# Optimization experiments

Hardware: AMD Instinct MI355X
Metric: run time of the kernel (lower is better)

## Reference

```python
import jax, jax.numpy as jnp
import numpy as np

N = 100_000      # nodes per type
E = 1_000_000    # edges per edge type
F_IN = 32        # raw feature dim
HID = 64         # hidden_channels
H, D = 2, 32     # num_heads, head_dim


def setup_inputs() -> dict:
    key = jax.random.key(0)
    ks = jax.random.split(key, 64)
    it = iter(range(64))
    def nrm(shape, scale=0.1):
        return jax.random.normal(ks[next(it)], shape, dtype=jnp.float32) * scale
    inp = {}
    inp['x_mac'] = jax.random.normal(ks[next(it)], (N, F_IN), dtype=jnp.float32)
    inp['x_buf'] = jax.random.normal(ks[next(it)], (N, F_IN), dtype=jnp.float32)
    inp['ei_m2b'] = jax.random.randint(ks[next(it)], (2, E), 0, N)
    inp['ei_b2m'] = jax.random.randint(ks[next(it)], (2, E), 0, N)
    for t in ('mac', 'buf'):
        inp[f'enc_w_{t}'] = nrm((F_IN, HID))
        inp[f'enc_b_{t}'] = jnp.zeros((HID,), jnp.float32)
        inp[f'enc_g_{t}'] = jnp.ones((HID,), jnp.float32)
        inp[f'enc_be_{t}'] = jnp.zeros((HID,), jnp.float32)
        for p in ('k', 'q', 'v'):
            inp[f'{p}_w_{t}'] = nrm((HID, HID))
            inp[f'{p}_b_{t}'] = jnp.zeros((HID,), jnp.float32)
        inp[f'o_w_{t}'] = nrm((HID, HID))
        inp[f'o_b_{t}'] = jnp.zeros((HID,), jnp.float32)
        inp[f'skip_{t}'] = jnp.ones((), jnp.float32)
    for r in ('m2b', 'b2m'):
        inp[f'a_{r}'] = nrm((H, D, D))
        inp[f'm_{r}'] = nrm((H, D, D))
        inp[f'p_{r}'] = jnp.ones((H,), jnp.float32)
    inp['ln_g'] = jnp.ones((HID,), jnp.float32)
    inp['ln_b'] = jnp.zeros((HID,), jnp.float32)
    return inp


def _ln(x, g, b, eps=1e-5):
    mu = jnp.mean(x, -1, keepdims=True)
    var = jnp.mean((x - mu) ** 2, -1, keepdims=True)
    return g * (x - mu) * jax.lax.rsqrt(var + eps) + b


def _seg_softmax(logits, seg, n):
    # logits: [E, H], seg: [E] dst ids. Numerically stable per-segment softmax.
    m = jax.ops.segment_max(logits, seg, num_segments=n)
    m = jnp.where(jnp.isfinite(m), m, 0.0)  # empty segments -> -inf
    e = jnp.exp(logits - m[seg])
    s = jax.ops.segment_sum(e, seg, num_segments=n)
    return e / (s[seg] + 1e-16)


def _hgt_edge(q_dst, k_src, v_src, a_rel, m_rel, p_rel, ei, n_dst):
    # q_dst:[Nd,H,D] k_src/v_src:[Ns,H,D] a_rel/m_rel:[H,D,D] p_rel:[H] ei:[2,E]
    src, dst = ei[0], ei[1]
    k = jnp.einsum('nhd,hde->nhe', k_src, a_rel)   # relation-transform keys
    v = jnp.einsum('nhd,hde->nhe', v_src, m_rel)   # relation-transform values
    alpha = (q_dst[dst] * k[src]).sum(-1) * p_rel / jnp.sqrt(jnp.float32(D))  # [E,H]
    alpha = _seg_softmax(alpha, dst, n_dst)
    msg = v[src] * alpha[..., None]                # [E,H,D]
    return jax.ops.segment_sum(msg, dst, num_segments=n_dst).reshape(n_dst, H * D)


def _forward(x_mac, x_buf, ei_m2b, ei_b2m,
             enc_w_mac, enc_b_mac, enc_g_mac, enc_be_mac,
             enc_w_buf, enc_b_buf, enc_g_buf, enc_be_buf,
             k_w_mac, k_b_mac, q_w_mac, q_b_mac, v_w_mac, v_b_mac,
             k_w_buf, k_b_buf, q_w_buf, q_b_buf, v_w_buf, v_b_buf,
             o_w_mac, o_b_mac, o_w_buf, o_b_buf, skip_mac, skip_buf,
             a_m2b, m_m2b, p_m2b, a_b2m, m_b2m, p_b2m, ln_g, ln_b):
    n_mac, n_buf = x_mac.shape[0], x_buf.shape[0]
    # per-type encoder: Linear -> LayerNorm -> ReLU (dropout = identity in eval)
    h_mac = jax.nn.relu(_ln(x_mac @ enc_w_mac + enc_b_mac, enc_g_mac, enc_be_mac))
    h_buf = jax.nn.relu(_ln(x_buf @ enc_w_buf + enc_b_buf, enc_g_buf, enc_be_buf))
    # HGTConv: per-type k/q/v projections -> [N,H,D]
    k_mac = (h_mac @ k_w_mac + k_b_mac).reshape(n_mac, H, D)
    q_mac = (h_mac @ q_w_mac + q_b_mac).reshape(n_mac, H, D)
    v_mac = (h_mac @ v_w_mac + v_b_mac).reshape(n_mac, H, D)
    k_buf = (h_buf @ k_w_buf + k_b_buf).reshape(n_buf, H, D)
    q_buf = (h_buf @ q_w_buf + q_b_buf).reshape(n_buf, H, D)
    v_buf = (h_buf @ v_w_buf + v_b_buf).reshape(n_buf, H, D)
    # per-edge-type attention + scatter-softmax + sum aggregate
    agg_buf = _hgt_edge(q_buf, k_mac, v_mac, a_m2b, m_m2b, p_m2b, ei_m2b, n_buf)
    agg_mac = _hgt_edge(q_mac, k_buf, v_buf, a_b2m, m_b2m, p_b2m, ei_b2m, n_mac)
    # per-dst-type output: out_lin(gelu(agg)), sigmoid-skip gating with input
    a_mac = jax.nn.gelu(agg_mac, approximate=False) @ o_w_mac + o_b_mac
    a_buf = jax.nn.gelu(agg_buf, approximate=False) @ o_w_buf + o_b_buf
    g_mac = jax.nn.sigmoid(skip_mac)
    g_buf = jax.nn.sigmoid(skip_buf)
    conv_mac = g_mac * a_mac + (1.0 - g_mac) * h_mac
    conv_buf = g_buf * a_buf + (1.0 - g_buf) * h_buf
    # module-level residual + shared LayerNorm
    y_mac = _ln(conv_mac + h_mac, ln_g, ln_b)
    y_buf = _ln(conv_buf + h_buf, ln_g, ln_b)
    return y_mac, y_buf


def reference(x_mac, x_buf, ei_m2b, ei_b2m,
              enc_w_mac, enc_b_mac, enc_g_mac, enc_be_mac,
              enc_w_buf, enc_b_buf, enc_g_buf, enc_be_buf,
              k_w_mac, k_b_mac, q_w_mac, q_b_mac, v_w_mac, v_b_mac,
              k_w_buf, k_b_buf, q_w_buf, q_b_buf, v_w_buf, v_b_buf,
              o_w_mac, o_b_mac, o_w_buf, o_b_buf, skip_mac, skip_buf,
              a_m2b, m_m2b, p_m2b, a_b2m, m_b2m, p_b2m, ln_g, ln_b):
    return _forward(x_mac, x_buf, ei_m2b, ei_b2m,
                    enc_w_mac, enc_b_mac, enc_g_mac, enc_be_mac,
                    enc_w_buf, enc_b_buf, enc_g_buf, enc_be_buf,
                    k_w_mac, k_b_mac, q_w_mac, q_b_mac, v_w_mac, v_b_mac,
                    k_w_buf, k_b_buf, q_w_buf, q_b_buf, v_w_buf, v_b_buf,
                    o_w_mac, o_b_mac, o_w_buf, o_b_buf, skip_mac, skip_buf,
                    a_m2b, m_m2b, p_m2b, a_b2m, m_b2m, p_b2m, ln_g, ln_b)
```

## Files before the change

kernel.cpp:

```cpp
#include <hip/hip_runtime.h>
#include <hip/hip_bf16.h>
#include <math.h>

#define NN 100000
#define NN2 200000
#define NE 1000000
#define FIN 32
#define HIDC 64

#define NB 782
#define NBP 1024
#define EPB 4096
#define SCGRID 489
#define CAP 3072
#define MAXIT 12
#define KQV_BLKS 1563

typedef unsigned int u32;
typedef unsigned short u16;

__device__ __forceinline__ float wsum(float v) {
  #pragma unroll
  for (int off = 32; off; off >>= 1) v += __shfl_xor(v, off, 64);
  return v;
}

__device__ __forceinline__ u16 f2bf(float f) {
  union { float f; u32 u; } c; c.f = f;
  u32 u = c.u;
  return (u16)((u + 0x7FFFu + ((u >> 16) & 1u)) >> 16);
}

__device__ __forceinline__ float bf2f(u32 v) {
  union { u32 u; float f; } c; c.u = v << 16; return c.f;
}

__device__ __forceinline__ void scan1024(u32* a, u32* wtot) {
  int t = threadIdx.x, lane = t & 63, wv = t >> 6;
  u32 v0 = a[t * 4 + 0], v1 = a[t * 4 + 1], v2 = a[t * 4 + 2], v3 = a[t * 4 + 3];
  u32 sum = v0 + v1 + v2 + v3;
  u32 x = sum;
  #pragma unroll
  for (int off = 1; off < 64; off <<= 1) {
    u32 y = __shfl_up(x, off, 64);
    if (lane >= off) x += y;
  }
  if (lane == 63) wtot[wv] = x;
  u32 excl = x - sum;
  __syncthreads();
  u32 wb = 0;
  #pragma unroll
  for (int w = 0; w < 4; w++) if (w < wv) wb += wtot[w];
  u32 b = wb + excl;
  a[t * 4 + 0] = b;
  a[t * 4 + 1] = b + v0;
  a[t * 4 + 2] = b + v0 + v1;
  a[t * 4 + 3] = b + v0 + v1 + v2;
}

__device__ __forceinline__ void edge_decode(
    int ee, const int* __restrict__ ei_m2b, const int* __restrict__ ei_b2m,
    int& src_g, int& dst_g) {
  if (ee < NE) {
    src_g = ei_m2b[ee];
    dst_g = NN + ei_m2b[NE + ee];
  } else {
    int e2 = ee - NE;
    src_g = NN + ei_b2m[e2];
    dst_g = ei_b2m[NE + e2];
  }
}

#define FUSE_T (64 * 192 + 192)
__global__ __launch_bounds__(256) void k_fuse(
    const float* __restrict__ qw0, const float* __restrict__ qb0,
    const float* __restrict__ kw0, const float* __restrict__ kb0,
    const float* __restrict__ vw0, const float* __restrict__ vb0,
    const float* __restrict__ ar0, const float* __restrict__ mr0,
    const float* __restrict__ p0,
    const float* __restrict__ qw1, const float* __restrict__ qb1,
    const float* __restrict__ kw1, const float* __restrict__ kb1,
    const float* __restrict__ vw1, const float* __restrict__ vb1,
    const float* __restrict__ ar1, const float* __restrict__ mr1,
    const float* __restrict__ p1,
    float* __restrict__ Wf, float* __restrict__ bfv) {
  int gidx = blockIdx.x * 256 + threadIdx.x;
  if (gidx >= 2 * FUSE_T) return;
  int type = gidx >= FUSE_T;
  int idx = gidx - type * FUSE_T;
  const float* qw = type ? qw1 : qw0; const float* qb = type ? qb1 : qb0;
  const float* kw = type ? kw1 : kw0; const float* kb = type ? kb1 : kb0;
  const float* vw = type ? vw1 : vw0; const float* vb = type ? vb1 : vb0;
  const float* ar = type ? ar1 : ar0; const float* mr = type ? mr1 : mr0;
  const float* p  = type ? p1  : p0;
  float* W = Wf + (size_t)type * 64 * 192;
  float* B = bfv + (size_t)type * 192;
  if (idx < 64 * 192) {
    int i = idx / 192, c = idx % 192;
    float o;
    if (c < 64) {
      o = qw[i * 64 + c];
    } else {
      int e = c & 63, hd = e >> 5, ee = e & 31;
      bool isK = c < 128;
      const float* M = isK ? ar : mr;
      const float* Wsrc = isK ? kw : vw;
      float s = 0.0f;
      #pragma unroll
      for (int d = 0; d < 32; ++d)
        s += Wsrc[i * 64 + hd * 32 + d] * M[hd * 32 * 32 + d * 32 + ee];
      if (isK) s *= p[hd] * 0.17677669529663687f;
      o = s;
    }
    W[i * 192 + c] = o;
  } else {
    int c = idx - 64 * 192;
    float o;
    if (c < 64) {
      o = qb[c];
    } else {
      int e = c & 63, hd = e >> 5, ee = e & 31;
      bool isK = c < 128;
      const float* M = isK ? ar : mr;
      const float* Bb = isK ? kb : vb;
      float s = 0.0f;
      #pragma unroll
      for (int d = 0; d < 32; ++d)
        s += Bb[hd * 32 + d] * M[hd * 32 * 32 + d * 32 + ee];
      if (isK) s *= p[hd] * 0.17677669529663687f;
      o = s;
    }
    B[c] = o;
  }
}

__global__ __launch_bounds__(256) void k_enc3(
    const float* __restrict__ x_mac, const float* __restrict__ x_buf,
    const float* __restrict__ w_mac, const float* __restrict__ b_mac,
    const float* __restrict__ g_mac, const float* __restrict__ be_mac,
    const float* __restrict__ w_buf, const float* __restrict__ b_buf,
    const float* __restrict__ g_buf, const float* __restrict__ be_buf,
    u16* __restrict__ hb) {
  __shared__ float xs[64][FIN + 1];
  __shared__ float ts[64][HIDC + 1];
  int t = threadIdx.x;
  int b = blockIdx.x;
  int type = b >= KQV_BLKS;
  int r0   = type ? (NN + (b - KQV_BLKS) * 64) : (b * 64);
  int rend = type ? NN2 : NN;
  const float* w  = type ? w_buf  : w_mac;
  const float* bb = type ? b_buf  : b_mac;
  const float* g  = type ? g_buf  : g_mac;
  const float* be = type ? be_buf : be_mac;
  const float* x  = type ? x_buf  : x_mac;
  int xoff = type ? NN : 0;
  for (int i = t; i < 64 * 8; i += 256) {
    int row = i >> 3, c4 = i & 7;
    int gr = r0 + row; if (gr >= rend) gr = rend - 1;
    float4 v = *(const float4*)&x[(size_t)(gr - xoff) * FIN + c4 * 4];
    xs[row][c4 * 4 + 0] = v.x; xs[row][c4 * 4 + 1] = v.y;
    xs[row][c4 * 4 + 2] = v.z; xs[row][c4 * 4 + 3] = v.w;
  }
  __syncthreads();
  int rg = t & 15, cg = t >> 4;
  float acc[4][4];
  #pragma unroll
  for (int c = 0; c < 4; c++) {
    float bv = bb[cg * 4 + c];
    #pragma unroll
    for (int r = 0; r < 4; r++) acc[r][c] = bv;
  }
  for (int k = 0; k < FIN; ++k) {
    float a0 = xs[rg * 4 + 0][k];
    float a1 = xs[rg * 4 + 1][k];
    float a2 = xs[rg * 4 + 2][k];
    float a3 = xs[rg * 4 + 3][k];
    float4 wv4 = *(const float4*)&w[k * HIDC + cg * 4];
    acc[0][0] = fmaf(a0, wv4.x, acc[0][0]); acc[0][1] = fmaf(a0, wv4.y, acc[0][1]);
    acc[0][2] = fmaf(a0, wv4.z, acc[0][2]); acc[0][3] = fmaf(a0, wv4.w, acc[0][3]);
    acc[1][0] = fmaf(a1, wv4.x, acc[1][0]); acc[1][1] = fmaf(a1, wv4.y, acc[1][1]);
    acc[1][2] = fmaf(a1, wv4.z, acc[1][2]); acc[1][3] = fmaf(a1, wv4.w, acc[1][3]);
    acc[2][0] = fmaf(a2, wv4.x, acc[2][0]); acc[2][1] = fmaf(a2, wv4.y, acc[2][1]);
    acc[2][2] = fmaf(a2, wv4.z, acc[2][2]); acc[2][3] = fmaf(a2, wv4.w, acc[2][3]);
    acc[3][0] = fmaf(a3, wv4.x, acc[3][0]); acc[3][1] = fmaf(a3, wv4.y, acc[3][1]);
    acc[3][2] = fmaf(a3, wv4.z, acc[3][2]); acc[3][3] = fmaf(a3, wv4.w, acc[3][3]);
  }
  #pragma unroll
  for (int r = 0; r < 4; r++)
    #pragma unroll
    for (int c = 0; c < 4; c++) ts[rg * 4 + r][cg * 4 + c] = acc[r][c];
  __syncthreads();
  int wv = t >> 6, ln = t & 63;
  for (int rr = wv; rr < 64; rr += 4) {
    int gr = r0 + rr;
    if (gr >= rend) break;
    float v = ts[rr][ln];
    float mu = wsum(v) * (1.0f / HIDC);
    float d = v - mu;
    float var = wsum(d * d) * (1.0f / HIDC);
    float yv = g[ln] * d * rsqrtf(var + 1e-5f) + be[ln];
    hb[(size_t)gr * HIDC + ln] = f2bf(fmaxf(yv, 0.0f));
  }
}

__global__ __launch_bounds__(256) void k_kqv3(
    const u16* __restrict__ hb, const float* __restrict__ Wf,
    const float* __restrict__ bfv,
    u16* __restrict__ qo, u32* __restrict__ kvt) {
  __shared__ float ws_[64 * 192];
  __shared__ float hs[64][65];
  int t = threadIdx.x;
  int b = blockIdx.x;
  int type = b >= KQV_BLKS;
  int r0   = type ? (NN + (b - KQV_BLKS) * 64) : (b * 64);
  int rend = type ? NN2 : NN;
  const float* W = Wf + (size_t)type * 64 * 192;
  const float* B = bfv + (size_t)type * 192;
  for (int i = t; i < 64 * 192 / 4; i += 256)
    ((float4*)ws_)[i] = ((const float4*)W)[i];
  for (int i = t; i < 64 * 8; i += 256) {
    int row = i >> 3, c8 = i & 7;
    int gr = r0 + row; if (gr >= rend) gr = rend - 1;
    uint4 v = *(const uint4*)&hb[(size_t)gr * 64 + c8 * 8];
    u32 a[4] = { v.x, v.y, v.z, v.w };
    #pragma unroll
    for (int j = 0; j < 4; j++) {
      hs[row][c8 * 8 + j * 2]     = bf2f(a[j] & 0xFFFFu);
      hs[row][c8 * 8 + j * 2 + 1] = bf2f(a[j] >> 16);
    }
  }
  __syncthreads();
  int rg = t & 15, cg = t >> 4;
  float acc[3][4][4];
  #pragma unroll
  for (int j = 0; j < 3; j++) {
    #pragma unroll
    for (int c = 0; c < 4; c++) {
      float bv = B[j * 64 + cg * 4 + c];
      #pragma unroll
      for (int r = 0; r < 4; r++) acc[j][r][c] = bv;
    }
  }
  for (int k = 0; k < 64; ++k) {
    float a0 = hs[rg * 4 + 0][k];
    float a1 = hs[rg * 4 + 1][k];
    float a2 = hs[rg * 4 + 2][k];
    float a3 = hs[rg * 4 + 3][k];
    #pragma unroll
    for (int j = 0; j < 3; j++) {
      float4 w = *(const float4*)&ws_[k * 192 + j * 64 + cg * 4];
      acc[j][0][0] = fmaf(a0, w.x, acc[j][0][0]);
      acc[j][0][1] = fmaf(a0, w.y, acc[j][0][1]);
      acc[j][0][2] = fmaf(a0, w.z, acc[j][0][2]);
      acc[j][0][3] = fmaf(a0, w.w, acc[j][0][3]);
      acc[j][1][0] = fmaf(a1, w.x, acc[j][1][0]);
      acc[j][1][1] = fmaf(a1, w.y, acc[j][1][1]);
      acc[j][1][2] = fmaf(a1, w.z, acc[j][1][2]);
      acc[j][1][3] = fmaf(a1, w.w, acc[j][1][3]);
      acc[j][2][0] = fmaf(a2, w.x, acc[j][2][0]);
      acc[j][2][1] = fmaf(a2, w.y, acc[j][2][1]);
      acc[j][2][2] = fmaf(a2, w.z, acc[j][2][2]);
      acc[j][2][3] = fmaf(a2, w.w, acc[j][2][3]);
      acc[j][3][0] = fmaf(a3, w.x, acc[j][3][0]);
      acc[j][3][1] = fmaf(a3, w.y, acc[j][3][1]);
      acc[j][3][2] = fmaf(a3, w.z, acc[j][3][2]);
      acc[j][3][3] = fmaf(a3, w.w, acc[j][3][3]);
    }
  }
  #pragma unroll
  for (int r = 0; r < 4; ++r) {
    int gr = r0 + rg * 4 + r;
    if (gr >= rend) break;
    u32 q0 = (u32)f2bf(acc[0][r][0]) | ((u32)f2bf(acc[0][r][1]) << 16);
    u32 q1 = (u32)f2bf(acc[0][r][2]) | ((u32)f2bf(acc[0][r][3]) << 16);
    *(u32*)&qo[(size_t)gr * 64 + cg * 4]     = q0;
    *(u32*)&qo[(size_t)gr * 64 + cg * 4 + 2] = q1;
    #pragma unroll
    for (int c = 0; c < 4; ++c) {
      u32 kv = (u32)f2bf(acc[1][r][c]) | ((u32)f2bf(acc[2][r][c]) << 16);
      kvt[(size_t)gr * 64 + cg * 4 + c] = kv;
    }
  }
}

__global__ __launch_bounds__(256) void k_out3(
    const u16* __restrict__ aggb, const u16* __restrict__ hb,
    const float* __restrict__ ow0, const float* __restrict__ ob0,
    const float* __restrict__ skip0,
    const float* __restrict__ ow1, const float* __restrict__ ob1,
    const float* __restrict__ skip1,
    const float* __restrict__ lg, const float* __restrict__ lb,
    float* __restrict__ y) {
  __shared__ float gs[64][65];
  int t = threadIdx.x;
  int b = blockIdx.x;
  int type = b >= KQV_BLKS;
  int r0   = type ? (NN + (b - KQV_BLKS) * 64) : (b * 64);
  int rend = type ? NN2 : NN;
  const float* ow = type ? ow1 : ow0;
  const float* ob = type ? ob1 : ob0;
  float gk = 1.0f / (1.0f + expf(-(type ? skip1 : skip0)[0]));
  for (int i = t; i < 64 * 8; i += 256) {
    int row = i >> 3, c8 = i & 7;
    int gr = r0 + row; if (gr >= rend) gr = rend - 1;
    uint4 v = *(const uint4*)&aggb[(size_t)gr * 64 + c8 * 8];
    u32 a[4] = { v.x, v.y, v.z, v.w };
    #pragma unroll
    for (int j = 0; j < 4; j++) {
      float f0 = bf2f(a[j] & 0xFFFFu);
      float f1 = bf2f(a[j] >> 16);
      gs[row][c8 * 8 + j * 2]     = 0.5f * f0 * (1.0f + erff(f0 * 0.70710678118654752f));
      gs[row][c8 * 8 + j * 2 + 1] = 0.5f * f1 * (1.0f + erff(f1 * 0.70710678118654752f));
    }
  }
  __syncthreads();
  int rg = t & 15, cg = t >> 4;
  float acc[4][4];
  #pragma unroll
  for (int c = 0; c < 4; c++) {
    float bv = ob[cg * 4 + c];
    #pragma unroll
    for (int r = 0; r < 4; r++) acc[r][c] = bv;
  }
  for (int k = 0; k < 64; ++k) {
    float a0 = gs[rg * 4 + 0][k];
    float a1 = gs[rg * 4 + 1][k];
    float a2 = gs[rg * 4 + 2][k];
    float a3 = gs[rg * 4 + 3][k];
    float4 wv4 = *(const float4*)&ow[k * 64 + cg * 4];
    acc[0][0] = fmaf(a0, wv4.x, acc[0][0]); acc[0][1] = fmaf(a0, wv4.y, acc[0][1]);
    acc[0][2] = fmaf(a0, wv4.z, acc[0][2]); acc[0][3] = fmaf(a0, wv4.w, acc[0][3]);
    acc[1][0] = fmaf(a1, wv4.x, acc[1][0]); acc[1][1] = fmaf(a1, wv4.y, acc[1][1]);
    acc[1][2] = fmaf(a1, wv4.z, acc[1][2]); acc[1][3] = fmaf(a1, wv4.w, acc[1][3]);
    acc[2][0] = fmaf(a2, wv4.x, acc[2][0]); acc[2][1] = fmaf(a2, wv4.y, acc[2][1]);
    acc[2][2] = fmaf(a2, wv4.z, acc[2][2]); acc[2][3] = fmaf(a2, wv4.w, acc[2][3]);
    acc[3][0] = fmaf(a3, wv4.x, acc[3][0]); acc[3][1] = fmaf(a3, wv4.y, acc[3][1]);
    acc[3][2] = fmaf(a3, wv4.z, acc[3][2]); acc[3][3] = fmaf(a3, wv4.w, acc[3][3]);
  }
  float tv[4][4];
  float c2 = 2.0f - gk;
  #pragma unroll
  for (int r = 0; r < 4; r++) {
    int gr = r0 + rg * 4 + r; if (gr >= rend) gr = rend - 1;
    uint2 hv = *(const uint2*)&hb[(size_t)gr * 64 + cg * 4];
    float h0 = bf2f(hv.x & 0xFFFFu), h1 = bf2f(hv.x >> 16);
    float h2 = bf2f(hv.y & 0xFFFFu), h3 = bf2f(hv.y >> 16);
    tv[r][0] = fmaf(gk, acc[r][0], c2 * h0);
    tv[r][1] = fmaf(gk, acc[r][1], c2 * h1);
    tv[r][2] = fmaf(gk, acc[r][2], c2 * h2);
    tv[r][3] = fmaf(gk, acc[r][3], c2 * h3);
  }
  __syncthreads();
  #pragma unroll
  for (int r = 0; r < 4; r++)
    #pragma unroll
    for (int c = 0; c < 4; c++) gs[rg * 4 + r][cg * 4 + c] = tv[r][c];
  __syncthreads();
  int wv = t >> 6, ln = t & 63;
  for (int rr = wv; rr < 64; rr += 4) {
    int gr = r0 + rr;
    if (gr >= rend) break;
    float v = gs[rr][ln];
    float mu = wsum(v) * (1.0f / HIDC);
    float d = v - mu;
    float var = wsum(d * d) * (1.0f / HIDC);
    y[(size_t)gr * HIDC + ln] = lg[ln] * d * rsqrtf(var + 1e-5f) + lb[ln];
  }
}

__global__ __launch_bounds__(256) void k_bscatter2(
    const int* __restrict__ ei_m2b, const int* __restrict__ ei_b2m,
    u32* __restrict__ gcursor, u32* __restrict__ bpairs) {
  __shared__ u32 hist[NBP];
  __shared__ u32 loff[NBP];
  __shared__ u32 gbase[NBP];
  __shared__ u32 wtot[4];
  __shared__ u32 pairs[EPB];
  __shared__ u16 sbuck[EPB];
  int tid = threadIdx.x;
  for (int i = tid; i < NBP; i += 256) hist[i] = 0;
  __syncthreads();
  int base_e = blockIdx.x * EPB;
  u32 pk[EPB / 256];
  u16 bk[EPB / 256];
  u16 rk[EPB / 256];
  #pragma unroll
  for (int i = 0; i < EPB / 256; i++) {
    int ee = base_e + i * 256 + tid;
    if (ee < 2 * NE) {
      int src_g, dst_g;
      edge_decode(ee, ei_m2b, ei_b2m, src_g, dst_g);
      u32 b = (u32)dst_g >> 8;
      pk[i] = ((u32)(dst_g & 255) << 18) | (u32)src_g;
      bk[i] = (u16)b;
      rk[i] = (u16)atomicAdd(&hist[b], 1u);
    } else {
      bk[i] = 0xFFFFu;
    }
  }
  __syncthreads();
  for (int i = tid; i < NBP; i += 256) loff[i] = hist[i];
  __syncthreads();
  scan1024(loff, wtot);
  __syncthreads();
  #pragma unroll
  for (int i = 0; i < EPB / 256; i++) {
    if (bk[i] != 0xFFFFu) {
      u32 s = loff[bk[i]] + rk[i];
      pairs[s] = pk[i];
      sbuck[s] = bk[i];
    }
  }
  __syncthreads();
  for (int b = tid; b < NBP; b += 256) {
    u32 c = hist[b];
    gbase[b] = c ? atomicAdd(&gcursor[b], c) : 0u;
  }
  __syncthreads();
  int nval = 2 * NE - base_e;
  if (nval > EPB) nval = EPB;
  for (int s = tid; s < nval; s += 256) {
    u32 b = sbuck[s];
    u32 slot = gbase[b] + (s - loff[b]);
    if (slot < CAP) bpairs[(size_t)b * CAP + slot] = pairs[s];
  }
}

__global__ __launch_bounds__(256) void k_bedge3(
    const u32* __restrict__ gcursor, const u32* __restrict__ bpairs,
    const u16* __restrict__ q, const u32* __restrict__ kvt,
    u16* __restrict__ aggb) {
  __shared__ u32 srt[CAP];
  __shared__ u32 hist[64];
  __shared__ u32 rowptr[65];
  int tid = threadIdx.x;
  int b = blockIdx.x >> 2;
  u32 qr = blockIdx.x & 3;
  u32 cnt = gcursor[b];
  int n = (int)(cnt > CAP ? CAP : cnt);
  if (tid < 64) hist[tid] = 0;
  __syncthreads();
  u32 pk[MAXIT];
  #pragma unroll
  for (int it = 0; it < MAXIT; it++) {
    pk[it] = 0xFFFFFFFFu;
    int i = tid + it * 256;
    if (i < n) {
      u32 p = bpairs[(size_t)b * CAP + i];
      u32 ld = p >> 18;
      if ((ld >> 6) == qr) {
        atomicAdd(&hist[ld & 63], 1u);
        pk[it] = p;
      }
    }
  }
  __syncthreads();
  if (tid < 64) {
    u32 v = hist[tid];
    u32 x = v;
    #pragma unroll
    for (int off = 1; off < 64; off <<= 1) {
      u32 y = __shfl_up(x, off, 64);
      if (tid >= off) x += y;
    }
    rowptr[tid] = x - v;
    if (tid == 63) rowptr[64] = x;
  }
  __syncthreads();
  if (tid < 64) hist[tid] = rowptr[tid];
  __syncthreads();
  #pragma unroll
  for (int it = 0; it < MAXIT; it++) {
    u32 p = pk[it];
    if (p != 0xFFFFFFFFu) {
      u32 pos = atomicAdd(&hist[(p >> 18) & 63], 1u);
      srt[pos] = p & 0x3FFFFu;
    }
  }
  __syncthreads();
  int grp = tid >> 4, t = tid & 15;
  for (int ld = grp; ld < 64; ld += 16) {
    int dst_g = (b << 8) + ((int)qr << 6) + ld;
    if (dst_g >= NN2) continue;
    u32 j0 = rowptr[ld], j1 = rowptr[ld + 1];
    uint2 qp = *(const uint2*)&q[(size_t)dst_g * 64 + t * 4];
    float q0 = bf2f(qp.x & 0xFFFFu), q1 = bf2f(qp.x >> 16);
    float q2 = bf2f(qp.y & 0xFFFFu), q3 = bf2f(qp.y >> 16);
    float m = -1e30f, s = 0.0f;
    float a0 = 0.0f, a1 = 0.0f, a2 = 0.0f, a3 = 0.0f;
    u32 j = j0;
    for (; j + 2 <= j1; j += 2) {
      u32 s0 = srt[j], s1 = srt[j + 1];
      uint4 w0 = *(const uint4*)&kvt[(size_t)s0 * 64 + t * 4];
      uint4 w1 = *(const uint4*)&kvt[(size_t)s1 * 64 + t * 4];
      {
        float k0 = bf2f(w0.x & 0xFFFFu), v0 = bf2f(w0.x >> 16);
        float k1 = bf2f(w0.y & 0xFFFFu), v1 = bf2f(w0.y >> 16);
        float k2 = bf2f(w0.z & 0xFFFFu), v2 = bf2f(w0.z >> 16);
        float k3 = bf2f(w0.w & 0xFFFFu), v3 = bf2f(w0.w >> 16);
        float prod = fmaf(q3, k3, fmaf(q2, k2, fmaf(q1, k1, q0 * k0)));
        prod += __shfl_xor(prod, 1, 64);
        prod += __shfl_xor(prod, 2, 64);
        prod += __shfl_xor(prod, 4, 64);
        float mn = fmaxf(m, prod);
        float c = __expf(m - mn);
        float we = __expf(prod - mn);
        s = fmaf(s, c, we);
        a0 = fmaf(a0, c, we * v0);
        a1 = fmaf(a1, c, we * v1);
        a2 = fmaf(a2, c, we * v2);
        a3 = fmaf(a3, c, we * v3);
        m = mn;
      }
      {
        float k0 = bf2f(w1.x & 0xFFFFu), v0 = bf2f(w1.x >> 16);
        float k1 = bf2f(w1.y & 0xFFFFu), v1 = bf2f(w1.y >> 16);
        float k2 = bf2f(w1.z & 0xFFFFu), v2 = bf2f(w1.z >> 16);
        float k3 = bf2f(w1.w & 0xFFFFu), v3 = bf2f(w1.w >> 16);
        float prod = fmaf(q3, k3, fmaf(q2, k2, fmaf(q1, k1, q0 * k0)));
        prod += __shfl_xor(prod, 1, 64);
        prod += __shfl_xor(prod, 2, 64);
        prod += __shfl_xor(prod, 4, 64);
        float mn = fmaxf(m, prod);
        float c = __expf(m - mn);
        float we = __expf(prod - mn);
        s = fmaf(s, c, we);
        a0 = fmaf(a0, c, we * v0);
        a1 = fmaf(a1, c, we * v1);
        a2 = fmaf(a2, c, we * v2);
        a3 = fmaf(a3, c, we * v3);
        m = mn;
      }
    }
    if (j < j1) {
      u32 s0 = srt[j];
      uint4 w0 = *(const uint4*)&kvt[(size_t)s0 * 64 + t * 4];
      float k0 = bf2f(w0.x & 0xFFFFu), v0 = bf2f(w0.x >> 16);
      float k1 = bf2f(w0.y & 0xFFFFu), v1 = bf2f(w0.y >> 16);
      float k2 = bf2f(w0.z & 0xFFFFu), v2 = bf2f(w0.z >> 16);
      float k3 = bf2f(w0.w & 0xFFFFu), v3 = bf2f(w0.w >> 16);
      float prod = fmaf(q3, k3, fmaf(q2, k2, fmaf(q1, k1, q0 * k0)));
      prod += __shfl_xor(prod, 1, 64);
      prod += __shfl_xor(prod, 2, 64);
      prod += __shfl_xor(prod, 4, 64);
      float mn = fmaxf(m, prod);
      float c = __expf(m - mn);
      float we = __expf(prod - mn);
      s = fmaf(s, c, we);
      a0 = fmaf(a0, c, we * v0);
      a1 = fmaf(a1, c, we * v1);
      a2 = fmaf(a2, c, we * v2);
      a3 = fmaf(a3, c, we * v3);
      m = mn;
    }
    float inv = 1.0f / (s + 1e-16f);
    u32 o0 = (u32)f2bf(a0 * inv) | ((u32)f2bf(a1 * inv) << 16);
    u32 o1 = (u32)f2bf(a2 * inv) | ((u32)f2bf(a3 * inv) << 16);
    uint2 o = { o0, o1 };
    *(uint2*)&aggb[(size_t)dst_g * 64 + t * 4] = o;
  }
}

extern "C" void kernel_launch(void* const* d_in, const int* in_sizes, int n_in,
                              void* d_out, int out_size, void* d_ws, size_t ws_size,
                              hipStream_t stream) {
  const float* x_mac     = (const float*)d_in[0];
  const float* x_buf     = (const float*)d_in[1];
  const int*   ei_m2b    = (const int*)d_in[2];
  const int*   ei_b2m    = (const int*)d_in[3];
  const float* enc_w_mac = (const float*)d_in[4];
  const float* enc_b_mac = (const float*)d_in[5];
  const float* enc_g_mac = (const float*)d_in[6];
  const float* enc_be_mac= (const float*)d_in[7];
  const float* k_w_mac   = (const float*)d_in[8];
  const float* k_b_mac   = (const float*)d_in[9];
  const float* q_w_mac   = (const float*)d_in[10];
  const float* q_b_mac   = (const float*)d_in[11];
  const float* v_w_mac   = (const float*)d_in[12];
  const float* v_b_mac   = (const float*)d_in[13];
  const float* o_w_mac   = (const float*)d_in[14];
  const float* o_b_mac   = (const float*)d_in[15];
  const float* skip_mac  = (const float*)d_in[16];
  const float* enc_w_buf = (const float*)d_in[17];
  const float* enc_b_buf = (const float*)d_in[18];
  const float* enc_g_buf = (const float*)d_in[19];
  const float* enc_be_buf= (const float*)d_in[20];
  const float* k_w_buf   = (const float*)d_in[21];
  const float* k_b_buf   = (const float*)d_in[22];
  const float* q_w_buf   = (const float*)d_in[23];
  const float* q_b_buf   = (const float*)d_in[24];
  const float* v_w_buf   = (const float*)d_in[25];
  const float* v_b_buf   = (const float*)d_in[26];
  const float* o_w_buf   = (const float*)d_in[27];
  const float* o_b_buf   = (const float*)d_in[28];
  const float* skip_buf  = (const float*)d_in[29];
  const float* a_m2b     = (const float*)d_in[30];
  const float* m_m2b     = (const float*)d_in[31];
  const float* p_m2b     = (const float*)d_in[32];
  const float* a_b2m     = (const float*)d_in[33];
  const float* m_b2m     = (const float*)d_in[34];
  const float* p_b2m     = (const float*)d_in[35];
  const float* ln_g      = (const float*)d_in[36];
  const float* ln_b      = (const float*)d_in[37];

  char* ws = (char*)d_ws;
  size_t off = 0;
  auto take = [&](size_t bytes) -> char* {
    char* p = ws + off;
    off = (off + bytes + 255) & ~(size_t)255;
    return p;
  };
  u16*   hb      = (u16*)take((size_t)NN2 * HIDC * 2);
  u16*   aggb    = (u16*)take((size_t)NN2 * HIDC * 2);
  u16*   q       = (u16*)take((size_t)NN2 * HIDC * 2);
  u32*   kvt     = (u32*)take((size_t)NN2 * HIDC * 4);
  float* Wf      = (float*)take((size_t)2 * 64 * 192 * 4);
  float* bfv     = (float*)take((size_t)2 * 192 * 4);
  u32*   gcursor = (u32*)take((size_t)NBP * 4);
  u32*   bpairs  = (u32*)take((size_t)NB * CAP * 4);

  const int tile_grid = 2 * KQV_BLKS;
  const int fuse_grid = (2 * FUSE_T + 255) / 256;

  k_fuse<<<fuse_grid, 256, 0, stream>>>(
      q_w_mac, q_b_mac, k_w_mac, k_b_mac, v_w_mac, v_b_mac, a_m2b, m_m2b, p_m2b,
      q_w_buf, q_b_buf, k_w_buf, k_b_buf, v_w_buf, v_b_buf, a_b2m, m_b2m, p_b2m,
      Wf, bfv);
  hipMemsetAsync(gcursor, 0, (size_t)NBP * 4, stream);
  k_bscatter2<<<SCGRID, 256, 0, stream>>>(ei_m2b, ei_b2m, gcursor, bpairs);
  k_enc3<<<tile_grid, 256, 0, stream>>>(
      x_mac, x_buf,
      enc_w_mac, enc_b_mac, enc_g_mac, enc_be_mac,
      enc_w_buf, enc_b_buf, enc_g_buf, enc_be_buf, hb);
  k_kqv3<<<tile_grid, 256, 0, stream>>>(hb, Wf, bfv, q, kvt);
  k_bedge3<<<4 * NB, 256, 0, stream>>>(gcursor, bpairs, q, kvt, aggb);
  k_out3<<<tile_grid, 256, 0, stream>>>(
      aggb, hb, o_w_mac, o_b_mac, skip_mac, o_w_buf, o_b_buf, skip_buf,
      ln_g, ln_b, (float*)d_out);
}
```

Baseline: 292.7 us.

## Compute KQV projection with bf16 MFMA using pre-transposed bf16 fused weights

The fused Q/K/V weight matrix is now stored transposed and in bf16, and the KQV kernel computes the 64x192 projection per 64-row tile with mfma_f32_16x16x32_bf16 fragments loaded straight from global memory. This drops the 48KB shared-memory weight staging, the float conversion of activations and the scalar FMA loop. The gain is meant to come from less shared memory use and higher occupancy. The cost is rounding the fused weights to bf16, a small precision loss, and output stores that are now scattered 2-byte writes.

```diff
diff --git a/kernel.cpp b/kernel.cpp
--- a/kernel.cpp
+++ b/kernel.cpp
@@ -19,6 +19,9 @@
 typedef unsigned int u32;
 typedef unsigned short u16;
 
+typedef __attribute__((ext_vector_type(8))) short bf16x8;
+typedef __attribute__((ext_vector_type(4))) float f32x4;
+
 __device__ __forceinline__ float wsum(float v) {
   #pragma unroll
   for (int off = 32; off; off >>= 1) v += __shfl_xor(v, off, 64);
@@ -33,6 +36,11 @@
 
 __device__ __forceinline__ float bf2f(u32 v) {
   union { u32 u; float f; } c; c.u = v << 16; return c.f;
+}
+
+__device__ __forceinline__ bf16x8 ldfrag(const u16* p) {
+  uint4 v = *(const uint4*)p;
+  union { uint4 u; bf16x8 b; } c; c.u = v; return c.b;
 }
 
 __device__ __forceinline__ void scan1024(u32* a, u32* wtot) {
@@ -71,8 +79,8 @@
   }
 }
 
-#define FUSE_T (64 * 192 + 192)
-__global__ __launch_bounds__(256) void k_fuse(
+#define FUSE2_T (192 * 64 + 192)
+__global__ __launch_bounds__(256) void k_fuse2(
     const float* __restrict__ qw0, const float* __restrict__ qb0,
     const float* __restrict__ kw0, const float* __restrict__ kb0,
     const float* __restrict__ vw0, const float* __restrict__ vb0,
@@ -83,23 +91,21 @@
     const float* __restrict__ vw1, const float* __restrict__ vb1,
     const float* __restrict__ ar1, const float* __restrict__ mr1,
     const float* __restrict__ p1,
-    float* __restrict__ Wf, float* __restrict__ bfv) {
+    u16* __restrict__ WfTb, float* __restrict__ bfv) {
   int gidx = blockIdx.x * 256 + threadIdx.x;
-  if (gidx >= 2 * FUSE_T) return;
-  int type = gidx >= FUSE_T;
-  int idx = gidx - type * FUSE_T;
+  if (gidx >= 2 * FUSE2_T) return;
+  int type = gidx >= FUSE2_T;
+  int idx = gidx - type * FUSE2_T;
   const float* qw = type ? qw1 : qw0; const float* qb = type ? qb1 : qb0;
   const float* kw = type ? kw1 : kw0; const float* kb = type ? kb1 : kb0;
   const float* vw = type ? vw1 : vw0; const float* vb = type ? vb1 : vb0;
   const float* ar = type ? ar1 : ar0; const float* mr = type ? mr1 : mr0;
   const float* p  = type ? p1  : p0;
-  float* W = Wf + (size_t)type * 64 * 192;
-  float* B = bfv + (size_t)type * 192;
-  if (idx < 64 * 192) {
-    int i = idx / 192, c = idx % 192;
+  if (idx < 192 * 64) {
+    int c = idx >> 6, k = idx & 63;
     float o;
     if (c < 64) {
-      o = qw[i * 64 + c];
+      o = qw[k * 64 + c];
     } else {
       int e = c & 63, hd = e >> 5, ee = e & 31;
       bool isK = c < 128;
@@ -108,13 +114,13 @@
       float s = 0.0f;
       #pragma unroll
       for (int d = 0; d < 32; ++d)
-        s += Wsrc[i * 64 + hd * 32 + d] * M[hd * 32 * 32 + d * 32 + ee];
+        s += Wsrc[k * 64 + hd * 32 + d] * M[hd * 32 * 32 + d * 32 + ee];
       if (isK) s *= p[hd] * 0.17677669529663687f;
       o = s;
     }
-    W[i * 192 + c] = o;
+    WfTb[(size_t)type * 192 * 64 + c * 64 + k] = f2bf(o);
   } else {
-    int c = idx - 64 * 192;
+    int c = idx - 192 * 64;
     float o;
     if (c < 64) {
       o = qb[c];
@@ -130,7 +136,7 @@
       if (isK) s *= p[hd] * 0.17677669529663687f;
       o = s;
     }
-    B[c] = o;
+    bfv[(size_t)type * 192 + c] = o;
   }
 }
 
@@ -203,82 +209,55 @@
   }
 }
 
-__global__ __launch_bounds__(256) void k_kqv3(
-    const u16* __restrict__ hb, const float* __restrict__ Wf,
+__global__ __launch_bounds__(256) void k_kqv4(
+    const u16* __restrict__ hb, const u16* __restrict__ WfTb,
     const float* __restrict__ bfv,
     u16* __restrict__ qo, u32* __restrict__ kvt) {
-  __shared__ float ws_[64 * 192];
-  __shared__ float hs[64][65];
   int t = threadIdx.x;
   int b = blockIdx.x;
   int type = b >= KQV_BLKS;
   int r0   = type ? (NN + (b - KQV_BLKS) * 64) : (b * 64);
   int rend = type ? NN2 : NN;
-  const float* W = Wf + (size_t)type * 64 * 192;
+  const u16* WT = WfTb + (size_t)type * 192 * 64;
   const float* B = bfv + (size_t)type * 192;
-  for (int i = t; i < 64 * 192 / 4; i += 256)
-    ((float4*)ws_)[i] = ((const float4*)W)[i];
-  for (int i = t; i < 64 * 8; i += 256) {
-    int row = i >> 3, c8 = i & 7;
-    int gr = r0 + row; if (gr >= rend) gr = rend - 1;
-    uint4 v = *(const uint4*)&hb[(size_t)gr * 64 + c8 * 8];
-    u32 a[4] = { v.x, v.y, v.z, v.w };
-    #pragma unroll
-    for (int j = 0; j < 4; j++) {
-      hs[row][c8 * 8 + j * 2]     = bf2f(a[j] & 0xFFFFu);
-      hs[row][c8 * 8 + j * 2 + 1] = bf2f(a[j] >> 16);
-    }
-  }
-  __syncthreads();
-  int rg = t & 15, cg = t >> 4;
-  float acc[3][4][4];
-  #pragma unroll
-  for (int j = 0; j < 3; j++) {
-    #pragma unroll
-    for (int c = 0; c < 4; c++) {
-      float bv = B[j * 64 + cg * 4 + c];
-      #pragma unroll
-      for (int r = 0; r < 4; r++) acc[j][r][c] = bv;
-    }
-  }
-  for (int k = 0; k < 64; ++k) {
-    float a0 = hs[rg * 4 + 0][k];
-    float a1 = hs[rg * 4 + 1][k];
-    float a2 = hs[rg * 4 + 2][k];
-    float a3 = hs[rg * 4 + 3][k];
-    #pragma unroll
-    for (int j = 0; j < 3; j++) {
-      float4 w = *(const float4*)&ws_[k * 192 + j * 64 + cg * 4];
-      acc[j][0][0] = fmaf(a0, w.x, acc[j][0][0]);
-      acc[j][0][1] = fmaf(a0, w.y, acc[j][0][1]);
-      acc[j][0][2] = fmaf(a0, w.z, acc[j][0][2]);
-      acc[j][0][3] = fmaf(a0, w.w, acc[j][0][3]);
-      acc[j][1][0] = fmaf(a1, w.x, acc[j][1][0]);
-      acc[j][1][1] = fmaf(a1, w.y, acc[j][1][1]);
-      acc[j][1][2] = fmaf(a1, w.z, acc[j][1][2]);
-      acc[j][1][3] = fmaf(a1, w.w, acc[j][1][3]);
-      acc[j][2][0] = fmaf(a2, w.x, acc[j][2][0]);
-      acc[j][2][1] = fmaf(a2, w.y, acc[j][2][1]);
-      acc[j][2][2] = fmaf(a2, w.z, acc[j][2][2]);
-      acc[j][2][3] = fmaf(a2, w.w, acc[j][2][3]);
-      acc[j][3][0] = fmaf(a3, w.x, acc[j][3][0]);
-      acc[j][3][1] = fmaf(a3, w.y, acc[j][3][1]);
-      acc[j][3][2] = fmaf(a3, w.z, acc[j][3][2]);
-      acc[j][3][3] = fmaf(a3, w.w, acc[j][3][3]);
-    }
-  }
-  #pragma unroll
-  for (int r = 0; r < 4; ++r) {
-    int gr = r0 + rg * 4 + r;
-    if (gr >= rend) break;
-    u32 q0 = (u32)f2bf(acc[0][r][0]) | ((u32)f2bf(acc[0][r][1]) << 16);
-    u32 q1 = (u32)f2bf(acc[0][r][2]) | ((u32)f2bf(acc[0][r][3]) << 16);
-    *(u32*)&qo[(size_t)gr * 64 + cg * 4]     = q0;
-    *(u32*)&qo[(size_t)gr * 64 + cg * 4 + 2] = q1;
-    #pragma unroll
-    for (int c = 0; c < 4; ++c) {
-      u32 kv = (u32)f2bf(acc[1][r][c]) | ((u32)f2bf(acc[2][r][c]) << 16);
-      kvt[(size_t)gr * 64 + cg * 4 + c] = kv;
+  int w = t >> 6, l = t & 63;
+  int lr = l & 15, lk = l >> 4;
+  int arow = r0 + w * 16 + lr;
+  int arowc = arow >= rend ? rend - 1 : arow;
+  bf16x8 a0 = ldfrag(&hb[(size_t)arowc * 64 + lk * 8]);
+  bf16x8 a1 = ldfrag(&hb[(size_t)arowc * 64 + 32 + lk * 8]);
+  f32x4 acc[12];
+  #pragma unroll
+  for (int j = 0; j < 12; j++) {
+    bf16x8 b0 = ldfrag(&WT[(size_t)(j * 16 + lr) * 64 + lk * 8]);
+    bf16x8 b1 = ldfrag(&WT[(size_t)(j * 16 + lr) * 64 + 32 + lk * 8]);
+    f32x4 c = {0.0f, 0.0f, 0.0f, 0.0f};
+    c = __builtin_amdgcn_mfma_f32_16x16x32_bf16(a0, b0, c, 0, 0, 0);
+    c = __builtin_amdgcn_mfma_f32_16x16x32_bf16(a1, b1, c, 0, 0, 0);
+    acc[j] = c;
+  }
+  int orow0 = r0 + w * 16 + lk * 4;
+  #pragma unroll
+  for (int j = 0; j < 4; j++) {
+    float bv = B[j * 16 + lr];
+    #pragma unroll
+    for (int r = 0; r < 4; r++) {
+      int orow = orow0 + r;
+      if (orow < rend)
+        qo[(size_t)orow * 64 + j * 16 + lr] = f2bf(acc[j][r] + bv);
+    }
+  }
+  #pragma unroll
+  for (int j = 0; j < 4; j++) {
+    float bk = B[64 + j * 16 + lr];
+    float bv2 = B[128 + j * 16 + lr];
+    #pragma unroll
+    for (int r = 0; r < 4; r++) {
+      int orow = orow0 + r;
+      if (orow < rend) {
+        u32 kv = (u32)f2bf(acc[4 + j][r] + bk) | ((u32)f2bf(acc[8 + j][r] + bv2) << 16);
+        kvt[(size_t)orow * 64 + j * 16 + lr] = kv;
+      }
     }
   }
 }
@@ -614,25 +593,25 @@
   u16*   aggb    = (u16*)take((size_t)NN2 * HIDC * 2);
   u16*   q       = (u16*)take((size_t)NN2 * HIDC * 2);
   u32*   kvt     = (u32*)take((size_t)NN2 * HIDC * 4);
-  float* Wf      = (float*)take((size_t)2 * 64 * 192 * 4);
+  u16*   WfTb    = (u16*)take((size_t)2 * 192 * 64 * 2);
   float* bfv     = (float*)take((size_t)2 * 192 * 4);
   u32*   gcursor = (u32*)take((size_t)NBP * 4);
   u32*   bpairs  = (u32*)take((size_t)NB * CAP * 4);
 
-  const int tile_grid = 2 * KQV_BLKS;
-  const int fuse_grid = (2 * FUSE_T + 255) / 256;
-
-  k_fuse<<<fuse_grid, 256, 0, stream>>>(
+  const int tile_grid  = 2 * KQV_BLKS;
+  const int fuse2_grid = (2 * FUSE2_T + 255) / 256;
+
+  k_fuse2<<<fuse2_grid, 256, 0, stream>>>(
       q_w_mac, q_b_mac, k_w_mac, k_b_mac, v_w_mac, v_b_mac, a_m2b, m_m2b, p_m2b,
       q_w_buf, q_b_buf, k_w_buf, k_b_buf, v_w_buf, v_b_buf, a_b2m, m_b2m, p_b2m,
-      Wf, bfv);
+      WfTb, bfv);
   hipMemsetAsync(gcursor, 0, (size_t)NBP * 4, stream);
   k_bscatter2<<<SCGRID, 256, 0, stream>>>(ei_m2b, ei_b2m, gcursor, bpairs);
   k_enc3<<<tile_grid, 256, 0, stream>>>(
       x_mac, x_buf,
       enc_w_mac, enc_b_mac, enc_g_mac, enc_be_mac,
       enc_w_buf, enc_b_buf, enc_g_buf, enc_be_buf, hb);
-  k_kqv3<<<tile_grid, 256, 0, stream>>>(hb, Wf, bfv, q, kvt);
+  k_kqv4<<<tile_grid, 256, 0, stream>>>(hb, WfTb, bfv, q, kvt);
   k_bedge3<<<4 * NB, 256, 0, stream>>>(gcursor, bpairs, q, kvt, aggb);
   k_out3<<<tile_grid, 256, 0, stream>>>(
       aggb, hb, o_w_mac, o_b_mac, skip_mac, o_w_buf, o_b_buf, skip_buf,
```

New measurement: 279.1 us. 1.05x faster.
